# Kernel tuning notes

Hardware: AMD Instinct MI355X
Metric: run time of the kernel (lower is better)

Reference implementation:

```python
import jax, jax.numpy as jnp
import numpy as np
from jax import lax

NEG = -1e30  # safe -inf surrogate (avoids nan grads)
CTC_WEIGHT = 0.3


def _excl_cumsum(e):
    # exclusive cumsum along last axis: (..., U) -> (..., U+1)
    c = jnp.cumsum(e, axis=-1)
    return jnp.concatenate([jnp.zeros_like(c[..., :1]), c], axis=-1)


def _rnnt_loss(log_probs, targets, frame_len, tgt_len, blank):
    """RNNT forward DP. log_probs: (B,T,U+1,V) log-softmaxed. Returns per-seq NLL (B,)."""
    B, T, U1, V = log_probs.shape
    blank_lp = log_probs[..., blank]  # (B,T,U1)
    emit = jnp.take_along_axis(log_probs[:, :, :U1 - 1, :],
                               targets[:, None, :, None], axis=3)[..., 0]  # (B,T,U)
    # alpha[0,u] = sum_{j<u} emit[0,j]
    alpha0 = _excl_cumsum(emit[:, 0])  # (B,U1)

    def step(alpha_prev, inp):
        blank_prev, emit_t = inp  # (B,U1), (B,U)
        a = alpha_prev + blank_prev
        # alpha[t,u] = LSE(a_u, alpha[t,u-1] + emit[t,u-1]) solved in closed form:
        # alpha[t,u] = E[u] + cumLSE_{k<=u}(a_k - E[k]),  E = exclusive cumsum of emit
        E = _excl_cumsum(emit_t)
        alpha_t = E + lax.associative_scan(jnp.logaddexp, a - E, axis=-1)
        return alpha_t, alpha_t

    xs = (jnp.swapaxes(blank_lp[:, :-1], 0, 1), jnp.swapaxes(emit[:, 1:], 0, 1))
    _, alphas = lax.scan(step, alpha0, xs)
    alphas = jnp.concatenate([alpha0[None], alphas], axis=0)  # (T,B,U1)
    bi = jnp.arange(B)
    t_idx = frame_len - 1
    ll = alphas[t_idx, bi, tgt_len] + blank_lp[bi, t_idx, tgt_len]
    return -ll


def _ctc_loss(log_probs, targets, frame_len, tgt_len, blank):
    """CTC forward DP. log_probs: (B,T,V) log-softmaxed. Returns per-seq NLL (B,)."""
    B, T, V = log_probs.shape
    U = targets.shape[1]
    S = 2 * U + 1
    ext = jnp.full((B, S), blank, dtype=targets.dtype).at[:, 1::2].set(targets)  # (B,S)
    lp_ext = jnp.take_along_axis(log_probs, ext[:, None, :], axis=2)  # (B,T,S)
    ext_m2 = jnp.pad(ext[:, :-2], ((0, 0), (2, 0)), constant_values=blank)
    can_skip = (jnp.arange(S)[None, :] >= 2) & (ext != blank) & (ext != ext_m2)
    alpha0 = jnp.full((B, S), NEG).at[:, 0].set(lp_ext[:, 0, 0]).at[:, 1].set(lp_ext[:, 0, 1])

    def step(alpha, lp_t):
        p1 = jnp.pad(alpha[:, :-1], ((0, 0), (1, 0)), constant_values=NEG)
        p2 = jnp.where(can_skip,
                       jnp.pad(alpha[:, :-2], ((0, 0), (2, 0)), constant_values=NEG), NEG)
        m = jnp.maximum(jnp.maximum(alpha, p1), p2)
        new = lp_t + m + jnp.log(jnp.exp(alpha - m) + jnp.exp(p1 - m) + jnp.exp(p2 - m))
        return new, new

    _, alphas = lax.scan(step, alpha0, jnp.swapaxes(lp_ext, 0, 1)[1:])
    alphas = jnp.concatenate([alpha0[None], alphas], axis=0)  # (T,B,S)
    bi = jnp.arange(B)
    t_idx = frame_len - 1
    a_last = alphas[t_idx, bi, 2 * tgt_len]
    a_prev = alphas[t_idx, bi, 2 * tgt_len - 1]
    return -jnp.logaddexp(a_last, a_prev)


def setup_inputs() -> dict:
    key = jax.random.key(0)
    ks = jax.random.split(key, 9)
    B, T, U, V = 4, 200, 50, 1024
    D, H = 512, 640
    return {
        "x_enc": jax.random.normal(ks[0], (B, T, D), jnp.float32),
        "x_dec": jax.random.normal(ks[1], (B, U + 1, H), jnp.float32),
        "target": jax.random.randint(ks[2], (B, U), 0, V - 1),  # excludes blank = V-1
        "frame_length": jax.random.randint(ks[3], (B,), 150, T + 1).astype(jnp.int32),
        "target_length": jax.random.randint(ks[4], (B,), 30, U + 1).astype(jnp.int32),
        "W_ctc": jax.random.normal(ks[5], (D, V), jnp.float32) * 0.02,
        "b_ctc": jnp.zeros((V,), jnp.float32),
        "W_enc": jax.random.normal(ks[6], (D, H), jnp.float32) * 0.02,
        "W_pred": jax.random.normal(ks[7], (H, H), jnp.float32) * 0.02,
        "b_joint": jnp.zeros((H,), jnp.float32),
        "W_out": jax.random.normal(ks[8], (H, V), jnp.float32) * 0.02,
        "b_out": jnp.zeros((V,), jnp.float32),
    }


def reference(x_enc, x_dec, target, frame_length, target_length,
              W_ctc, b_ctc, W_enc, W_pred, b_joint, W_out, b_out):
    B = x_enc.shape[0]
    V = W_ctc.shape[1]
    blank = V - 1
    # CTC head: linear + log_softmax over vocab
    ctc_lp = jax.nn.log_softmax(x_enc @ W_ctc + b_ctc, axis=-1)  # (B,T,V)
    # Joiner: enc proj (B,T,1,J) + pred proj (B,1,U+1,J) -> tanh -> vocab
    joint = jnp.tanh(jnp.einsum('btd,dj->btj', x_enc, W_enc)[:, :, None, :]
                     + jnp.einsum('buh,hj->buj', x_dec, W_pred)[:, None, :, :]
                     + b_joint)  # (B,T,U+1,J)
    rnnt_lp = jax.nn.log_softmax(jnp.einsum('btuj,jv->btuv', joint, W_out) + b_out, axis=-1)
    rnnt = _rnnt_loss(rnnt_lp, target, frame_length, target_length, blank).mean()
    ctc = _ctc_loss(ctc_lp, target, frame_length, target_length, blank).sum() / B
    return rnnt + CTC_WEIGHT * ctc
```

## Files before the change

kernel.cpp:

```cpp
#include <hip/hip_runtime.h>
#include <hip/hip_bf16.h>

typedef __bf16 bf16_t;
typedef __attribute__((ext_vector_type(8))) __bf16 bf16x8;
typedef __attribute__((ext_vector_type(4))) float f32x4;
typedef __attribute__((ext_vector_type(8))) int i32x8;
typedef __attribute__((ext_vector_type(4))) int i32x4;

#define NEGV (-1e30f)

#define BB 4
#define TT 200
#define UU 50
#define U1 51
#define VV 1024
#define DD 512
#define HH 640
#define RTOT (BB*TT*U1)
#define RPAD 40832
#define SS 101

__device__ __forceinline__ float lae(float a, float b) {
    float mx = fmaxf(a, b);
    return mx + __logf(__expf(a - mx) + __expf(b - mx));
}
__device__ __forceinline__ float lae3(float a, float b, float c) {
    float mx = fmaxf(fmaxf(a, b), c);
    return mx + __logf(__expf(a - mx) + __expf(b - mx) + __expf(c - mx));
}
__device__ __forceinline__ float tanh_fast(float x) {
    float ex = __expf(2.f * x);
    return 1.f - 2.f / (ex + 1.f);
}

__device__ __forceinline__ void pack_seg(const float* __restrict__ W, bf16_t* __restrict__ Wf,
                                         int e, int K32, int N)
{
    int j  = e & 7;
    int l  = (e >> 3) & 63;
    int kk = (e >> 9) % K32;
    int nt = e / (K32 * 512);
    int v = nt * 16 + (l & 15);
    int k = kk * 32 + ((l >> 4) << 2) + (j & 3) + ((j >> 2) << 4);
    Wf[e] = (bf16_t)W[(size_t)k * N + v];
}

__device__ __forceinline__ void pack_out8_mx(const float* __restrict__ W, unsigned* __restrict__ Wf8,
                                             int e32)
{
    int w4   = e32 & 7;
    int l    = (e32 >> 3) & 63;
    int ksnt = e32 >> 9;
    int ks   = ksnt % 5;
    int nt   = ksnt / 5;
    int v = nt * 16 + (l & 15);
    int kb = ks * 128 + ((l >> 4) << 5) + w4 * 4;
    float f[4];
#pragma unroll
    for (int t = 0; t < 4; ++t) f[t] = W[(size_t)(kb + t) * VV + v] * 16.f;
    unsigned r = __builtin_amdgcn_cvt_pk_fp8_f32(f[0], f[1], 0, false);
    r = __builtin_amdgcn_cvt_pk_fp8_f32(f[2], f[3], r, true);
    Wf8[e32] = r;
}

__global__ void pack_all(const float* __restrict__ Wout, const float* __restrict__ Wenc,
                         const float* __restrict__ Wpred, const float* __restrict__ Wctc,
                         unsigned* __restrict__ FOut8, bf16_t* __restrict__ FEnc,
                         bf16_t* __restrict__ FPred, bf16_t* __restrict__ FCtc)
{
    int e = blockIdx.x * 256 + threadIdx.x;
    if (e < 163840) { pack_out8_mx(Wout, FOut8, e); return; }
    e -= 163840;
    if (e < 327680) { pack_seg(Wenc, FEnc, e, 16, 640); return; }
    e -= 327680;
    if (e < 409600) { pack_seg(Wpred, FPred, e, 20, 640); return; }
    e -= 409600;
    pack_seg(Wctc, FCtc, e, 16, 1024);
}

template<int K32, int L, bool LSE, int J>
__device__ void gemm_dev(const float* __restrict__ A, int M, int rowbase, int K,
                         const bf16_t* __restrict__ Wf, const float* __restrict__ bias,
                         float* __restrict__ C, float* __restrict__ lse_out, int N,
                         bf16_t* Atile, float (*ps)[8])
{
    const int tid = threadIdx.x;
#pragma unroll
    for (int it = 0; it < J * K32 / 8; ++it) {
        int fi = it * 512 + tid;
        int l = fi & 63, jk = fi >> 6;
        int j = jk / K32, kk = jk - j * K32;
        int row = rowbase + j * 16 + (l & 15);
        if (row > M - 1) row = M - 1;
        int c0 = kk * 32 + ((l >> 4) << 2);
        const float4 a0 = *(const float4*)&A[(size_t)row * K + c0];
        const float4 a1 = *(const float4*)&A[(size_t)row * K + c0 + 16];
        bf16x8 v;
        v[0] = (bf16_t)a0.x; v[1] = (bf16_t)a0.y; v[2] = (bf16_t)a0.z; v[3] = (bf16_t)a0.w;
        v[4] = (bf16_t)a1.x; v[5] = (bf16_t)a1.y; v[6] = (bf16_t)a1.z; v[7] = (bf16_t)a1.w;
        *(bf16x8*)&Atile[(size_t)fi * 8] = v;
    }
    __syncthreads();

    const int l = tid & 63, w = tid >> 6;
    const int lrow = l & 15, lhi = l >> 4;

    f32x4 acc[J][L];
#pragma unroll
    for (int j = 0; j < J; ++j)
#pragma unroll
        for (int li = 0; li < L; ++li) acc[j][li] = f32x4{0.f, 0.f, 0.f, 0.f};

    for (int kk = 0; kk < K32; ++kk) {
        bf16x8 a[J];
#pragma unroll
        for (int j = 0; j < J; ++j)
            a[j] = *(const bf16x8*)&Atile[(size_t)(((j * K32 + kk) * 64 + l) * 8)];
#pragma unroll
        for (int li = 0; li < L; ++li) {
            bf16x8 b = *(const bf16x8*)&Wf[(size_t)(((w * L + li) * K32 + kk) * 64 + l) * 8];
#pragma unroll
            for (int j = 0; j < J; ++j)
                acc[j][li] = __builtin_amdgcn_mfma_f32_16x16x32_bf16(a[j], b, acc[j][li], 0, 0, 0);
        }
    }

    float se[J][4];
    if (LSE) {
#pragma unroll
        for (int j = 0; j < J; ++j)
#pragma unroll
            for (int i = 0; i < 4; ++i) se[j][i] = 0.f;
    }
#pragma unroll
    for (int j = 0; j < J; ++j)
#pragma unroll
        for (int li = 0; li < L; ++li) {
            int col = (w * L + li) * 16 + lrow;
            float bv = bias ? bias[col] : 0.f;
#pragma unroll
            for (int i = 0; i < 4; ++i) {
                int grow = rowbase + 16 * j + lhi * 4 + i;
                float x = acc[j][li][i] + bv;
                if (grow < M) C[(size_t)grow * N + col] = x;
                if (LSE) se[j][i] += __expf(x);
            }
        }
    if (LSE) {
#pragma unroll
        for (int d = 1; d < 16; d <<= 1)
#pragma unroll
            for (int j = 0; j < J; ++j)
#pragma unroll
                for (int i = 0; i < 4; ++i) se[j][i] += __shfl_xor(se[j][i], d);
        if (lrow == 0) {
#pragma unroll
            for (int j = 0; j < J; ++j)
#pragma unroll
                for (int i = 0; i < 4; ++i) ps[16 * j + lhi * 4 + i][w] = se[j][i];
        }
        __syncthreads();
        if (tid < J * 16) {
            float s = 0.f;
#pragma unroll
            for (int w0 = 0; w0 < 8; ++w0) s += ps[tid][w0];
            int grow = rowbase + tid;
            if (grow < M) lse_out[grow] = __logf(s);
        }
    }
}

__global__ __launch_bounds__(512)
void mfma_gemm3(const float* __restrict__ x_enc, const float* __restrict__ x_dec,
                const bf16_t* __restrict__ FEnc, const bf16_t* __restrict__ FPred,
                const bf16_t* __restrict__ FCtc, const float* __restrict__ b_ctc,
                float* __restrict__ enc_proj, float* __restrict__ pred_proj,
                float* __restrict__ ctc_logits, float* __restrict__ ctc_lse)
{
    __shared__ bf16_t Atile[40960];
    __shared__ float ps[64][8];
    int blk = blockIdx.x;
    if (blk < 13)
        gemm_dev<16, 5, false, 4>(x_enc, 800, blk * 64, 512, FEnc, nullptr, enc_proj, nullptr, 640, Atile, ps);
    else if (blk < 17)
        gemm_dev<20, 5, false, 4>(x_dec, 204, (blk - 13) * 64, 640, FPred, nullptr, pred_proj, nullptr, 640, Atile, ps);
    else
        gemm_dev<16, 8, true, 4>(x_enc, 800, (blk - 17) * 64, 512, FCtc, b_ctc, ctc_logits, ctc_lse, 1024, Atile, ps);
}

__global__ __launch_bounds__(512)
void joint_gemm(const float* __restrict__ enc,
                const float* __restrict__ pred,
                const float* __restrict__ bj,
                const unsigned* __restrict__ Wf8,
                const float* __restrict__ bo,
                const int* __restrict__ target,
                float* __restrict__ blank_buf, float* __restrict__ emit_buf)
{
    __shared__ __align__(16) char smbuf[40960];
    char* Afrag8 = smbuf;
    const int tid = threadIdx.x;
    const int blk = blockIdx.x;

    const int l = tid & 63, w = tid >> 6;
    const int lrow = l & 15, lhi = l >> 4;

#pragma unroll
    for (int it = 0; it < 5; ++it) {
        int c = it * 512 + tid;
        int lA = c & 63;
        int plane = c >> 6;
        int h = plane & 1;
        int jks = plane >> 1;
        int ks = jks % 5;
        int j = jks / 5;
        int row = j * 16 + (lA & 15);
        int r = blk * 64 + row; if (r > RTOT - 1) r = RTOT - 1;
        int b = r / (TT * U1); int rem = r - b * (TT * U1);
        int t = rem / U1;      int u = rem - t * U1;
        const float* erow = enc + (size_t)(b * TT + t) * HH;
        const float* prow = pred + (size_t)(b * U1 + u) * HH;
        int c0 = ks * 128 + ((lA >> 4) << 5) + h * 16;
        float f[16];
#pragma unroll
        for (int s = 0; s < 4; ++s) {
            int off = c0 + s * 4;
            const float4 e4 = *(const float4*)&erow[off];
            const float4 p4 = *(const float4*)&prow[off];
            const float4 q4 = *(const float4*)&bj[off];
            f[s * 4 + 0] = tanh_fast(e4.x + p4.x + q4.x);
            f[s * 4 + 1] = tanh_fast(e4.y + p4.y + q4.y);
            f[s * 4 + 2] = tanh_fast(e4.z + p4.z + q4.z);
            f[s * 4 + 3] = tanh_fast(e4.w + p4.w + q4.w);
        }
        uint4 v;
        unsigned r0 = __builtin_amdgcn_cvt_pk_fp8_f32(f[0], f[1], 0, false);
        v.x = __builtin_amdgcn_cvt_pk_fp8_f32(f[2], f[3], r0, true);
        r0 = __builtin_amdgcn_cvt_pk_fp8_f32(f[4], f[5], 0, false);
        v.y = __builtin_amdgcn_cvt_pk_fp8_f32(f[6], f[7], r0, true);
        r0 = __builtin_amdgcn_cvt_pk_fp8_f32(f[8], f[9], 0, false);
        v.z = __builtin_amdgcn_cvt_pk_fp8_f32(f[10], f[11], r0, true);
        r0 = __builtin_amdgcn_cvt_pk_fp8_f32(f[12], f[13], 0, false);
        v.w = __builtin_amdgcn_cvt_pk_fp8_f32(f[14], f[15], r0, true);
        *(uint4*)&Afrag8[(size_t)c * 16] = v;
    }
    __syncthreads();

    f32x4 acc[4][8];
#pragma unroll
    for (int j = 0; j < 4; ++j)
#pragma unroll
        for (int li = 0; li < 8; ++li) acc[j][li] = f32x4{0.f, 0.f, 0.f, 0.f};

    const char* Bp8 = (const char*)Wf8 + (size_t)(w * 8) * 10240 + (size_t)l * 32;

    const int rot = blk % 5;
    auto kstep = [&](int ks) {
        i32x8 a[4];
#pragma unroll
        for (int j = 0; j < 4; ++j) {
            i32x4 lo = *(const i32x4*)(Afrag8 + (size_t)(((j * 5 + ks) * 2 + 0) * 1024 + l * 16));
            i32x4 hi = *(const i32x4*)(Afrag8 + (size_t)(((j * 5 + ks) * 2 + 1) * 1024 + l * 16));
            a[j][0] = lo[0]; a[j][1] = lo[1]; a[j][2] = lo[2]; a[j][3] = lo[3];
            a[j][4] = hi[0]; a[j][5] = hi[1]; a[j][6] = hi[2]; a[j][7] = hi[3];
        }
#pragma unroll
        for (int li = 0; li < 8; ++li) {
            i32x8 b = *(const i32x8*)(Bp8 + (size_t)li * 10240 + (size_t)ks * 2048);
#pragma unroll
            for (int j = 0; j < 4; ++j)
                acc[j][li] = __builtin_amdgcn_mfma_scale_f32_16x16x128_f8f6f4(
                    a[j], b, acc[j][li], 0, 0,
                    0, 0x7F7F7F7F, 0, 0x7F7F7F7F);
        }
    };
    for (int ks0 = rot; ks0 < 5; ++ks0) kstep(ks0);
    for (int ks0 = 0; ks0 < rot; ++ks0) kstep(ks0);

    int tg[4][4];
#pragma unroll
    for (int j = 0; j < 4; ++j)
#pragma unroll
        for (int i = 0; i < 4; ++i) {
            int r = blk * 64 + 16 * j + lhi * 4 + i; if (r > RTOT - 1) r = RTOT - 1;
            int b = r / (TT * U1); int rem = r - b * (TT * U1);
            int u = rem % U1;
            tg[j][i] = (u < UU) ? target[b * UU + u] : -1;
        }

    float se[4][4], ee[4][4], bbv[4][4];
#pragma unroll
    for (int j = 0; j < 4; ++j)
#pragma unroll
        for (int i = 0; i < 4; ++i) { se[j][i] = 0.f; ee[j][i] = NEGV; bbv[j][i] = NEGV; }

#pragma unroll
    for (int li = 0; li < 8; ++li) {
        int col = (w * 8 + li) * 16 + lrow;
        float bv = bo[col];
#pragma unroll
        for (int j = 0; j < 4; ++j)
#pragma unroll
            for (int i = 0; i < 4; ++i) {
                float x = acc[j][li][i] * 0.0625f + bv;
                se[j][i] += __expf(x);
                if (col == tg[j][i]) ee[j][i] = x;
            }
    }
    if (w == 7) {
        float bv = bo[1023];
#pragma unroll
        for (int j = 0; j < 4; ++j)
#pragma unroll
            for (int i = 0; i < 4; ++i) {
                float x = acc[j][7][i] * 0.0625f + bv;
                if (lrow == 15) bbv[j][i] = x;
            }
    }
#pragma unroll
    for (int d = 1; d < 16; d <<= 1)
#pragma unroll
        for (int j = 0; j < 4; ++j)
#pragma unroll
            for (int i = 0; i < 4; ++i) {
                se[j][i] += __shfl_xor(se[j][i], d);
                ee[j][i] = fmaxf(ee[j][i], __shfl_xor(ee[j][i], d));
                bbv[j][i] = fmaxf(bbv[j][i], __shfl_xor(bbv[j][i], d));
            }

    __syncthreads();
    float (*ps)[8] = (float (*)[8])(smbuf);
    float (*pe)[8] = (float (*)[8])(smbuf + 2048);
    float (*pb)[8] = (float (*)[8])(smbuf + 4096);
    if (lrow == 0) {
#pragma unroll
        for (int j = 0; j < 4; ++j)
#pragma unroll
            for (int i = 0; i < 4; ++i) {
                int r = 16 * j + lhi * 4 + i;
                ps[r][w] = se[j][i]; pe[r][w] = ee[j][i]; pb[r][w] = bbv[j][i];
            }
    }
    __syncthreads();
    if (tid < 64) {
        float s = 0.f, e = NEGV, bq = NEGV;
#pragma unroll
        for (int w0 = 0; w0 < 8; ++w0) {
            s += ps[tid][w0];
            e = fmaxf(e, pe[tid][w0]);
            bq = fmaxf(bq, pb[tid][w0]);
        }
        float lse = __logf(s);
        int gid = blk * 64 + tid;
        if (gid < RTOT) {
            blank_buf[gid] = bq - lse;
            emit_buf[gid]  = e - lse;
        }
    }
}

__global__ __launch_bounds__(256)
void dp_fused(const float* __restrict__ blank_buf, const float* __restrict__ emit_buf,
              const float* __restrict__ ctc_logits, const float* __restrict__ ctc_lse,
              const int* __restrict__ target, const int* __restrict__ frame_len,
              const int* __restrict__ tgt_len,
              float* __restrict__ loss_rnnt, float* __restrict__ loss_ctc)
{
    __shared__ __align__(16) float sm[28416];
    const int bid = blockIdx.x;
    const int tid = threadIdx.x;

    if (bid < 4) {
        const int b = bid;
        float2* pk = (float2*)sm;
        for (int i = tid; i < TT * U1; i += 256) {
            int t = i / U1, uu = i - t * U1;
            float bl = blank_buf[(b * TT + t) * U1 + uu];
            float em = emit_buf[(b * TT + t) * U1 + uu];
            pk[uu * 217 + t + 8] = make_float2(bl, em);
        }
        __syncthreads();
        if (tid >= 64) return;
        const int u = tid;
        const int fl = frame_len[b], tl = tgt_len[b];
        const int dh = fl - 1 + tl;
        const bool isTL = (u == tl);
        const bool act = (u < U1);
        float A = (u == 0) ? 0.f : NEGV;
        float Asave = (dh == 0 && isTL) ? A : NEGV;
        const float2* prow = pk + u * 217;

        for (int d0 = 1; d0 <= 249; d0 += 8) {
            int tb = d0 - 1 - u;
            int tc = tb; if (tc < -8) tc = -8; if (tc > 200) tc = 200;
            float2 buf[8];
#pragma unroll
            for (int s = 0; s < 8; ++s) buf[s] = prow[tc + 8 + s];
#pragma unroll
            for (int s = 0; s < 8; ++s) {
                int d = d0 + s;
                int t_new = d - u;
                float2 be = buf[s];
                float vshare = A + be.y;
                float left = __shfl_up(vshare, 1);
                if (u == 0) left = NEGV;
                float up = (t_new >= 1) ? (A + be.x) : NEGV;
                float Anew = lae(up, left);
                bool valid = act && (t_new >= 0) && (t_new < TT);
                A = valid ? Anew : A;
                Asave = (isTL && d == dh) ? A : Asave;
            }
        }
        if (isTL && act) {
            float bl = prow[(fl - 1) + 8].x;
            loss_rnnt[b] = -(Asave + bl);
        }
    } else {
        const int b = bid - 4;
        float* lpE = sm;
        float* lpO = sm + 208;
        for (int i = tid; i < TT; i += 256) {
            int bt = b * TT + i;
            lpE[i] = ctc_logits[(size_t)bt * VV + (VV - 1)] - ctc_lse[bt];
        }
        for (int i = tid; i < TT * UU; i += 256) {
            int t = i / UU, uu = i - t * UU;
            int bt = b * TT + t;
            lpO[uu * 209 + t] = ctc_logits[(size_t)bt * VV + target[b * UU + uu]] - ctc_lse[bt];
        }
        __syncthreads();
        if (tid >= 64) return;
        const int u = tid;
        const int fl = frame_len[b], tl = tgt_len[b];
        const bool acte = (u <= 50);
        const bool acto = (u < 50);
        bool skip = (u >= 1 && u < UU) ? (target[b * UU + u] != target[b * UU + u - 1]) : false;
        const float* orow = lpO + u * 209;
        float old_e = (u == 0) ? lpE[0] : NEGV;
        float old_o = (u == 0) ? orow[0] : NEGV;
        float Esave = (fl == 1) ? old_e : NEGV;
        float Osave = (fl == 1) ? old_o : NEGV;

        for (int t0 = 1; t0 <= 193; t0 += 8) {
            float bo8[8], be8[8];
#pragma unroll
            for (int s = 0; s < 8; ++s) { bo8[s] = orow[t0 + s]; be8[s] = lpE[t0 + s]; }
#pragma unroll
            for (int s = 0; s < 8; ++s) {
                int t = t0 + s;
                float prev_o = __shfl_up(old_o, 1);
                if (u == 0) prev_o = NEGV;
                float ne = be8[s] + lae(old_e, prev_o);
                float no = bo8[s] + lae3(old_o, old_e, skip ? prev_o : NEGV);
                old_e = acte ? ne : NEGV;
                old_o = acto ? no : NEGV;
                bool hv = (t == fl - 1) && (t < TT);
                Esave = hv ? old_e : Esave;
                Osave = hv ? old_o : Osave;
            }
        }
        float a_last = __shfl(Esave, tl);
        float a_prev = __shfl(Osave, tl - 1);
        if (u == 0) loss_ctc[b] = -lae(a_last, a_prev);
    }
}

__global__ void combine(const float* __restrict__ lr, const float* __restrict__ lc,
                        float* __restrict__ out)
{
    float r = 0.25f * (lr[0] + lr[1] + lr[2] + lr[3]);
    float c = 0.25f * (lc[0] + lc[1] + lc[2] + lc[3]);
    out[0] = r + 0.3f * c;
}

extern "C" void kernel_launch(void* const* d_in, const int* in_sizes, int n_in,
                              void* d_out, int out_size, void* d_ws, size_t ws_size,
                              hipStream_t stream)
{
    const float* x_enc   = (const float*)d_in[0];
    const float* x_dec   = (const float*)d_in[1];
    const int*   target  = (const int*)d_in[2];
    const int*   frame_l = (const int*)d_in[3];
    const int*   tgt_l   = (const int*)d_in[4];
    const float* W_ctc   = (const float*)d_in[5];
    const float* b_ctc   = (const float*)d_in[6];
    const float* W_enc   = (const float*)d_in[7];
    const float* W_pred  = (const float*)d_in[8];
    const float* b_joint = (const float*)d_in[9];
    const float* W_out   = (const float*)d_in[10];
    const float* b_out   = (const float*)d_in[11];
    float* out = (float*)d_out;

    float* wsf        = (float*)d_ws;
    float* enc_proj   = wsf;
    float* pred_proj  = wsf + 512000;
    float* ctc_logits = wsf + 642560;
    float* ctc_lse    = wsf + 1461760;
    float* blank_buf  = wsf + 1462592;
    float* emit_buf   = wsf + 1503424;
    float* loss_rnnt  = wsf + 1544256;
    float* loss_ctc   = wsf + 1544260;
    unsigned* FOut8 = (unsigned*)(wsf + 1544272);
    bf16_t* FEnc  = (bf16_t*)(wsf + 1708112);
    bf16_t* FPred = (bf16_t*)(wsf + 1871952);
    bf16_t* FCtc  = (bf16_t*)(wsf + 2076752);

    pack_all<<<5568, 256, 0, stream>>>(W_out, W_enc, W_pred, W_ctc, FOut8, FEnc, FPred, FCtc);
    mfma_gemm3<<<30, 512, 0, stream>>>(x_enc, x_dec, FEnc, FPred, FCtc, b_ctc,
                                       enc_proj, pred_proj, ctc_logits, ctc_lse);
    joint_gemm<<<RPAD / 64, 512, 0, stream>>>(enc_proj, pred_proj, b_joint, FOut8, b_out,
                                              target, blank_buf, emit_buf);
    dp_fused<<<8, 256, 0, stream>>>(blank_buf, emit_buf, ctc_logits, ctc_lse,
                                    target, frame_l, tgt_l, loss_rnnt, loss_ctc);
    combine<<<1, 1, 0, stream>>>(loss_rnnt, loss_ctc, out);
}
```

Measured before the change: 159.6 us.

## Split joint tanh/fp8 build into separate kernel and fold loss combine into atomics

Moves the tanh(enc+pred+bias) plus fp8 packing of the joint A-tile out of joint_gemm into a standalone build_joint kernel that writes pre-packed fragments to global memory. joint_gemm then only copies those fragments into LDS before the MFMA loop. The combine kernel is dropped: dp_fused atomically adds the scaled per-sequence losses into the output, which is zeroed by a memset. This trades a global round trip of about 26MB of fp8 data for a shorter, simpler GEMM prologue and one fewer launch.

```diff
diff --git a/kernel.cpp b/kernel.cpp
--- a/kernel.cpp
+++ b/kernel.cpp
@@ -18,6 +18,7 @@
 #define HH 640
 #define RTOT (BB*TT*U1)
 #define RPAD 40832
+#define NBLK 638
 #define SS 101
 
 __device__ __forceinline__ float lae(float a, float b) {
@@ -188,26 +189,15 @@
         gemm_dev<16, 8, true, 4>(x_enc, 800, (blk - 17) * 64, 512, FCtc, b_ctc, ctc_logits, ctc_lse, 1024, Atile, ps);
 }
 
-__global__ __launch_bounds__(512)
-void joint_gemm(const float* __restrict__ enc,
-                const float* __restrict__ pred,
-                const float* __restrict__ bj,
-                const unsigned* __restrict__ Wf8,
-                const float* __restrict__ bo,
-                const int* __restrict__ target,
-                float* __restrict__ blank_buf, float* __restrict__ emit_buf)
-{
-    __shared__ __align__(16) char smbuf[40960];
-    char* Afrag8 = smbuf;
+__global__ __launch_bounds__(256)
+void build_joint(const float* __restrict__ enc, const float* __restrict__ pred,
+                 const float* __restrict__ bj, char* __restrict__ FA8)
+{
+    const int blk = blockIdx.x;
     const int tid = threadIdx.x;
-    const int blk = blockIdx.x;
-
-    const int l = tid & 63, w = tid >> 6;
-    const int lrow = l & 15, lhi = l >> 4;
-
-#pragma unroll
-    for (int it = 0; it < 5; ++it) {
-        int c = it * 512 + tid;
+#pragma unroll
+    for (int it = 0; it < 10; ++it) {
+        int c = it * 256 + tid;
         int lA = c & 63;
         int plane = c >> 6;
         int h = plane & 1;
@@ -242,7 +232,30 @@
         v.z = __builtin_amdgcn_cvt_pk_fp8_f32(f[10], f[11], r0, true);
         r0 = __builtin_amdgcn_cvt_pk_fp8_f32(f[12], f[13], 0, false);
         v.w = __builtin_amdgcn_cvt_pk_fp8_f32(f[14], f[15], r0, true);
-        *(uint4*)&Afrag8[(size_t)c * 16] = v;
+        *(uint4*)&FA8[(size_t)blk * 40960 + (size_t)c * 16] = v;
+    }
+}
+
+__global__ __launch_bounds__(512)
+void joint_gemm(const char* __restrict__ FA8,
+                const unsigned* __restrict__ Wf8,
+                const float* __restrict__ bo,
+                const int* __restrict__ target,
+                float* __restrict__ blank_buf, float* __restrict__ emit_buf)
+{
+    __shared__ __align__(16) char smbuf[40960];
+    char* Afrag8 = smbuf;
+    const int tid = threadIdx.x;
+    const int blk = blockIdx.x;
+
+    const int l = tid & 63, w = tid >> 6;
+    const int lrow = l & 15, lhi = l >> 4;
+
+    const uint4* src = (const uint4*)(FA8 + (size_t)blk * 40960);
+#pragma unroll
+    for (int it = 0; it < 5; ++it) {
+        int c = it * 512 + tid;
+        *(uint4*)&Afrag8[(size_t)c * 16] = src[c];
     }
     __syncthreads();
 
@@ -364,7 +377,7 @@
               const float* __restrict__ ctc_logits, const float* __restrict__ ctc_lse,
               const int* __restrict__ target, const int* __restrict__ frame_len,
               const int* __restrict__ tgt_len,
-              float* __restrict__ loss_rnnt, float* __restrict__ loss_ctc)
+              float* __restrict__ out)
 {
     __shared__ __align__(16) float sm[28416];
     const int bid = blockIdx.x;
@@ -413,7 +426,7 @@
         }
         if (isTL && act) {
             float bl = prow[(fl - 1) + 8].x;
-            loss_rnnt[b] = -(Asave + bl);
+            atomicAdd(out, -0.25f * (Asave + bl));
         }
     } else {
         const int b = bid - 4;
@@ -461,16 +474,8 @@
         }
         float a_last = __shfl(Esave, tl);
         float a_prev = __shfl(Osave, tl - 1);
-        if (u == 0) loss_ctc[b] = -lae(a_last, a_prev);
-    }
-}
-
-__global__ void combine(const float* __restrict__ lr, const float* __restrict__ lc,
-                        float* __restrict__ out)
-{
-    float r = 0.25f * (lr[0] + lr[1] + lr[2] + lr[3]);
-    float c = 0.25f * (lc[0] + lc[1] + lc[2] + lc[3]);
-    out[0] = r + 0.3f * c;
+        if (u == 0) atomicAdd(out, -0.075f * lae(a_last, a_prev));
+    }
 }
 
 extern "C" void kernel_launch(void* const* d_in, const int* in_sizes, int n_in,
@@ -498,19 +503,18 @@
     float* ctc_lse    = wsf + 1461760;
     float* blank_buf  = wsf + 1462592;
     float* emit_buf   = wsf + 1503424;
-    float* loss_rnnt  = wsf + 1544256;
-    float* loss_ctc   = wsf + 1544260;
     unsigned* FOut8 = (unsigned*)(wsf + 1544272);
     bf16_t* FEnc  = (bf16_t*)(wsf + 1708112);
     bf16_t* FPred = (bf16_t*)(wsf + 1871952);
     bf16_t* FCtc  = (bf16_t*)(wsf + 2076752);
-
+    char*   FA8   = (char*)(wsf + 2338896);
+
+    hipMemsetAsync(out, 0, sizeof(float), stream);
     pack_all<<<5568, 256, 0, stream>>>(W_out, W_enc, W_pred, W_ctc, FOut8, FEnc, FPred, FCtc);
     mfma_gemm3<<<30, 512, 0, stream>>>(x_enc, x_dec, FEnc, FPred, FCtc, b_ctc,
                                        enc_proj, pred_proj, ctc_logits, ctc_lse);
-    joint_gemm<<<RPAD / 64, 512, 0, stream>>>(enc_proj, pred_proj, b_joint, FOut8, b_out,
-                                              target, blank_buf, emit_buf);
+    build_joint<<<NBLK, 256, 0, stream>>>(enc_proj, pred_proj, b_joint, FA8);
+    joint_gemm<<<NBLK, 512, 0, stream>>>(FA8, FOut8, b_out, target, blank_buf, emit_buf);
     dp_fused<<<8, 256, 0, stream>>>(blank_buf, emit_buf, ctc_logits, ctc_lse,
-                                    target, frame_l, tgt_l, loss_rnnt, loss_ctc);
-    combine<<<1, 1, 0, stream>>>(loss_rnnt, loss_ctc, out);
-}
+                                    target, frame_l, tgt_l, out);
+}
```

Measured after the change: 170.2 us. 1.07x slower.
